# Kernel optimization log

Hardware: AMD Instinct MI355X
Metric: run time of the kernel (lower is better)

The kernel has to match this reference:

```python
import jax, jax.numpy as jnp
from jax import lax
import numpy as np
import math

B_SZ, SEQ, D_MODEL = 2, 2048, 2048
D_INNER, D_STATE, D_CONV, HEADS, P, CHUNK = 4096, 128, 4, 64, 64, 128
CONV_DIM = D_INNER + 2 * D_STATE
D_IN_PROJ = 2 * D_INNER + 2 * D_STATE + HEADS


def setup_inputs() -> dict:
    key = jax.random.key(0)
    ks = jax.random.split(key, 6)
    hidden_states = jax.random.normal(ks[0], (B_SZ, SEQ, D_MODEL), jnp.float32)
    W_in = jax.random.normal(ks[1], (D_IN_PROJ, D_MODEL), jnp.float32) * 0.02
    W_conv = jax.random.normal(ks[2], (CONV_DIM, 1, D_CONV), jnp.float32) * 0.2
    b_conv = jnp.zeros((CONV_DIM,), jnp.float32)
    A_log = jnp.log(jnp.arange(1, HEADS + 1, dtype=jnp.float32))
    D = jnp.ones((HEADS,), jnp.float32)
    # dt_bias init as in the torch module
    dt = jnp.exp(jax.random.uniform(ks[3], (HEADS,)) * (math.log(0.1) - math.log(0.001)) + math.log(0.001))
    dt = jnp.clip(dt, 1e-4, None)
    dt_bias = dt + jnp.log(-jnp.expm1(-dt))
    norm_weight = jnp.ones((D_INNER,), jnp.float32)
    W_out = jax.random.normal(ks[4], (D_MODEL, D_INNER), jnp.float32) * 0.02
    return {"hidden_states": hidden_states, "W_in": W_in, "W_conv": W_conv, "b_conv": b_conv,
            "A_log": A_log, "D": D, "dt_bias": dt_bias, "norm_weight": norm_weight, "W_out": W_out}


def _mamba2_core(hidden_states, W_in, W_conv, b_conv, A_log, D, dt_bias, norm_weight, W_out):
    Bsz, L, _ = hidden_states.shape
    NC = L // CHUNK
    zxbcdt = hidden_states @ W_in.T                         # [B,L,d_in_proj]
    z = zxbcdt[..., :D_INNER]
    xBC = zxbcdt[..., D_INNER:D_INNER + CONV_DIM]
    dt = zxbcdt[..., -HEADS:]
    # causal depthwise conv1d over sequence
    xc = jnp.swapaxes(xBC, 1, 2)                            # [B,C,L]
    xc = lax.conv_general_dilated(xc, W_conv, (1,), [(D_CONV - 1, 0)],
                                  feature_group_count=CONV_DIM,
                                  dimension_numbers=('NCH', 'OIH', 'NCH'))
    xc = xc + b_conv[None, :, None]
    xBC = jax.nn.silu(jnp.swapaxes(xc, 1, 2))               # [B,L,conv_dim]
    x = xBC[..., :D_INNER]
    Bm = xBC[..., D_INNER:D_INNER + D_STATE]                # num_groups=1
    Cm = xBC[..., -D_STATE:]
    dt = jax.nn.softplus(dt + dt_bias)                      # [B,L,H]; dt_limit (0,inf) is a no-op
    A = -jnp.exp(A_log)                                     # [H]
    # --- chunked SSD scan (chunk_size = CHUNK), same math as torch_ssm ---
    xch = x.reshape(Bsz, NC, CHUNK, HEADS, P)
    dtc = dt.reshape(Bsz, NC, CHUNK, HEADS)
    Bc = Bm.reshape(Bsz, NC, CHUNK, D_STATE)
    Cc = Cm.reshape(Bsz, NC, CHUNK, D_STATE)
    u = xch * dtc[..., None]                                # [b,c,l,h,p]
    dA = dtc * A                                            # [b,c,l,h]
    dA_cs = jnp.cumsum(dA, axis=2)                          # [b,c,l,h]
    # within-chunk causal attention-like term
    seg = dA_cs[:, :, :, None, :] - dA_cs[:, :, None, :, :] # [b,c,l,s,h]
    mask = jnp.tril(jnp.ones((CHUNK, CHUNK), bool))
    Lmat = jnp.exp(jnp.where(mask[None, None, :, :, None], seg, -jnp.inf))
    CB = jnp.einsum('bcln,bcsn->bcls', Cc, Bc)
    M = CB[..., None] * Lmat                                # [b,c,l,s,h]
    Y_diag = jnp.einsum('bclsh,bcshp->bclhp', M, u)
    # per-chunk final states
    decay_states = jnp.exp(dA_cs[:, :, -1:, :] - dA_cs)     # [b,c,l,h]
    states = jnp.einsum('bcln,bclh,bclhp->bchpn', Bc, decay_states, u)
    chunk_decay = jnp.exp(dA_cs[:, :, -1, :])               # [b,c,h]
    # inter-chunk recurrence over NC chunks
    def step(h, inp):
        st, cd = inp                                        # [b,h,p,n], [b,h]
        h_new = h * cd[:, :, None, None] + st
        return h_new, h                                     # emit state at chunk start
    sts = jnp.moveaxis(states, 1, 0)
    cds = jnp.moveaxis(chunk_decay, 1, 0)
    h0 = jnp.zeros((Bsz, HEADS, P, D_STATE), hidden_states.dtype)
    _, h_starts = lax.scan(step, h0, (sts, cds))
    h_starts = jnp.moveaxis(h_starts, 0, 1)                 # [b,c,h,p,n]
    state_decay_out = jnp.exp(dA_cs)                        # [b,c,l,h]
    Y_off = jnp.einsum('bcln,bclh,bchpn->bclhp', Cc, state_decay_out, h_starts)
    Y = Y_diag + Y_off + D[None, None, None, :, None] * xch
    y = Y.reshape(Bsz, L, D_INNER)
    # gated RMSNorm (gate first, then norm; group_size == d_inner)
    yg = y * jax.nn.silu(z)
    var = jnp.mean(yg * yg, axis=-1, keepdims=True)
    y = yg * lax.rsqrt(var + 1e-5) * norm_weight
    return y @ W_out.T


def reference(hidden_states, W_in, W_conv, b_conv, A_log, D, dt_bias, norm_weight, W_out):
    return _mamba2_core(hidden_states, W_in, W_conv, b_conv, A_log, D, dt_bias, norm_weight, W_out)
```

## Files before the change

kernel.cpp:

```cpp
#include <hip/hip_runtime.h>
#include <hip/hip_bf16.h>
#include <stdint.h>

typedef __bf16 bf16;
typedef __bf16 bf16x8 __attribute__((ext_vector_type(8)));
typedef __bf16 bf16x4 __attribute__((ext_vector_type(4)));
typedef float f32x4v __attribute__((ext_vector_type(4)));

#define SEQ    2048
#define DMODEL 2048
#define DI     4096
#define NH     64
#define PDIM   64
#define CHUNKL 128
#define NCH    16
#define CONVD  4352
#define DPROJ  8512
#define ZLD    8704
#define NTOK   4096
#define LP     136

__device__ __forceinline__ float sigmoid_f(float x){ return 1.f/(1.f+expf(-x)); }
__device__ __forceinline__ float silu_f(float x){ return x*sigmoid_f(x); }
__device__ __forceinline__ float softplus_f(float x){ return x > 20.f ? x : log1pf(expf(x)); }

__global__ __launch_bounds__(256) void cvt_all_kernel(const float* __restrict__ hs,
                                                      const float* __restrict__ W_in,
                                                      const float* __restrict__ W_out,
                                                      bf16* __restrict__ hsb,
                                                      bf16* __restrict__ winb,
                                                      bf16* __restrict__ woutb){
    int blk = blockIdx.x;
    if (blk < 8192){
        int i = (blk*256 + threadIdx.x)*4;
        float4 v = *(const float4*)&hs[i];
        bf16x4 o; o[0]=(bf16)v.x; o[1]=(bf16)v.y; o[2]=(bf16)v.z; o[3]=(bf16)v.w;
        *(bf16x4*)&hsb[i] = o;
    } else if (blk < 25600){
        int i = ((blk-8192)*256 + threadIdx.x)*4;
        int r = i >> 11;
        bf16x4 o;
        if (r < DPROJ){
            float4 v = *(const float4*)&W_in[i];
            o[0]=(bf16)v.x; o[1]=(bf16)v.y; o[2]=(bf16)v.z; o[3]=(bf16)v.w;
        } else {
            o[0]=(bf16)0.f; o[1]=(bf16)0.f; o[2]=(bf16)0.f; o[3]=(bf16)0.f;
        }
        *(bf16x4*)&winb[i] = o;
    } else {
        int i = ((blk-25600)*256 + threadIdx.x)*4;
        float4 v = *(const float4*)&W_out[i];
        bf16x4 o; o[0]=(bf16)v.x; o[1]=(bf16)v.y; o[2]=(bf16)v.z; o[3]=(bf16)v.w;
        *(bf16x4*)&woutb[i] = o;
    }
}

#define READ_A(BUFP, QM)                                                               \
    {                                                                                  \
        _Pragma("unroll")                                                              \
        for (int i=0;i<4;i++)                                                          \
            _Pragma("unroll")                                                          \
            for (int k2=0;k2<2;k2++)                                                   \
                af[i][k2] = *(const bf16x8*)&(BUFP)[aoff[i][k2] + (QM)*8192];          \
    }

#define READ_B(BUFP, QN)                                                               \
    {                                                                                  \
        _Pragma("unroll")                                                              \
        for (int nf=0;nf<2;nf++)                                                       \
            _Pragma("unroll")                                                          \
            for (int k2=0;k2<2;k2++)                                                   \
                bfr[nf][k2] = *(const bf16x8*)&(BUFP)[boff[nf][k2] + (QN)*8192];       \
    }

#define MMA_Q(QM, QN)                                                                  \
    {                                                                                  \
        __builtin_amdgcn_s_setprio(1);                                                 \
        _Pragma("unroll")                                                              \
        for (int i=0;i<4;i++)                                                          \
            _Pragma("unroll")                                                          \
            for (int nf=0;nf<2;nf++)                                                   \
                _Pragma("unroll")                                                      \
                for (int k2=0;k2<2;k2++)                                               \
                    acc[(QM)*4+i][(QN)*2+nf] = __builtin_amdgcn_mfma_f32_16x16x32_bf16( \
                        af[i][k2], bfr[nf][k2], acc[(QM)*4+i][(QN)*2+nf], 0,0,0);      \
        __builtin_amdgcn_s_setprio(0);                                                 \
    }

#define SBAR() do { __builtin_amdgcn_sched_barrier(0);                                 \
                    __builtin_amdgcn_s_barrier();                                      \
                    asm volatile("s_waitcnt lgkmcnt(0)" ::: "memory");                 \
                    __builtin_amdgcn_sched_barrier(0); } while(0)
#define EBAR() do { __builtin_amdgcn_s_barrier();                                      \
                    __builtin_amdgcn_sched_barrier(0); } while(0)

template<int MODE>
__global__ __launch_bounds__(512) void gemm256_kernel(const bf16* __restrict__ A,
                                                      const bf16* __restrict__ Bmat,
                                                      void* __restrict__ Cout,
                                                      int NXB, int NYB, int K, int ldc){
    __shared__ __align__(16) bf16 lds[2][2*16384];
    const int tid  = threadIdx.x;
    const int w    = tid >> 6;
    const int lane = tid & 63;
    const int wm   = w >> 2, wn = w & 3;

    int bid = blockIdx.x;
    int x, y, kz = 0;
    if (MODE == 3){
        kz = bid >> 5;
        int t32 = bid & 31;
        x = 32 + (t32 & 1);
        y = t32 >> 1;
    } else {
        int nb2  = (int)gridDim.x;
        int wg   = (bid & 7)*(nb2 >> 3) + (bid >> 3);
        const int SW = 8;
        int sup = wg / (SW*NYB);
        int rr  = wg % (SW*NYB);
        int x0  = sup*SW;
        int wl  = (NXB - x0 < SW) ? (NXB - x0) : SW;
        x = x0 + rr % wl;
        y = rr / wl;
    }
    const int tm = y*256, tn = x*256;

    const int KT  = (MODE==3) ? 8 : (K >> 6);
    const int kt0 = kz * KT;

    f32x4v acc[8][4];
    #pragma unroll
    for (int i=0;i<8;i++)
        #pragma unroll
        for (int j=0;j<4;j++) acc[i][j] = {0.f,0.f,0.f,0.f};
    bf16x8 af[4][2];
    bf16x8 bfr[2][2];

    const bf16* srcA[2][2];
    const bf16* srcB[2][2];
    #pragma unroll
    for (int r0h=0;r0h<2;r0h++)
        #pragma unroll
        for (int i=0;i<2;i++){
            int lr = r0h*128 + i*64 + (tid>>3);
            int growA = tm + ((lr>>6)&1)*128 + (lr>>7)*64 + (lr&63);
            int growB = tn + ((lr>>5)&3)*64 + (lr>>7)*32 + (lr&31);
            int gslot = (tid&7) ^ (lr&7);
            srcA[r0h][i] = A + (long)growA*K + gslot*8;
            srcB[r0h][i] = Bmat + (long)growB*K + gslot*8;
        }
    int aoff[4][2], boff[2][2];
    #pragma unroll
    for (int i=0;i<4;i++)
        #pragma unroll
        for (int k2=0;k2<2;k2++){
            int ra0 = wm*64 + i*16 + (lane&15);
            int slot = (k2*4 + (lane>>4)) ^ (ra0&7);
            aoff[i][k2] = ra0*64 + slot*8;
        }
    #pragma unroll
    for (int nf=0;nf<2;nf++)
        #pragma unroll
        for (int k2=0;k2<2;k2++){
            int rb0 = wn*32 + nf*16 + (lane&15);
            int slot = (k2*4 + (lane>>4)) ^ (rb0&7);
            boff[nf][k2] = 16384 + rb0*64 + slot*8;
        }

    auto stageA = [&](int buf, int t, int r0h){
        long koff = (long)(kt0 + t)*64;
        #pragma unroll
        for (int i=0;i<2;i++){
            bf16* dst = &lds[buf][0] + (size_t)(r0h*128 + i*64 + w*8)*64;
            __builtin_amdgcn_global_load_lds(
                (const __attribute__((address_space(1))) void*)(srcA[r0h][i] + koff),
                (__attribute__((address_space(3))) void*)dst, 16, 0, 0);
        }
    };
    auto stageB = [&](int buf, int t, int r0h){
        long koff = (long)(kt0 + t)*64;
        #pragma unroll
        for (int i=0;i<2;i++){
            bf16* dst = &lds[buf][16384] + (size_t)(r0h*128 + i*64 + w*8)*64;
            __builtin_amdgcn_global_load_lds(
                (const __attribute__((address_space(1))) void*)(srcB[r0h][i] + koff),
                (__attribute__((address_space(3))) void*)dst, 16, 0, 0);
        }
    };

    stageA(0, 0, 0);
    stageB(0, 0, 0);
    stageA(0, 0, 1);
    stageB(0, 0, 1);
    if (KT > 1){ stageA(1, 1, 0); stageB(1, 1, 0); }
    asm volatile("s_waitcnt vmcnt(8)" ::: "memory");
    __builtin_amdgcn_s_barrier();

    int cur = 0;
    for (int t = 0; t < KT; ++t){
        int nxt = cur ^ 1;
        const bf16* bufc = &lds[cur][0];
        READ_A(bufc, 0)
        READ_B(bufc, 0)
        if (t+1 < KT){
            stageA(nxt, t+1, 1);
            asm volatile("s_waitcnt vmcnt(6)" ::: "memory");
        } else {
            asm volatile("s_waitcnt vmcnt(0)" ::: "memory");
        }
        SBAR();
        MMA_Q(0, 0)
        READ_B(bufc, 1)
        if (t+1 < KT) stageB(nxt, t+1, 1);
        SBAR();
        MMA_Q(0, 1)
        READ_A(bufc, 1)
        READ_B(bufc, 0)
        if (t+2 < KT) stageA(cur, t+2, 0);
        SBAR();
        MMA_Q(1, 0)
        EBAR();
        READ_B(bufc, 1)
        if (t+2 < KT){
            stageB(cur, t+2, 0);
            asm volatile("s_waitcnt vmcnt(8)" ::: "memory");
        } else {
            asm volatile("s_waitcnt vmcnt(4)" ::: "memory");
        }
        SBAR();
        MMA_Q(1, 1)
        cur = nxt;
    }

    const int er = (lane>>4)*4, ec = lane&15;
    #pragma unroll
    for (int mi=0;mi<8;mi++)
        #pragma unroll
        for (int ni=0;ni<4;ni++){
            long r0 = tm + wm*128 + mi*16 + er;
            int  c0 = tn + wn*64 + ni*16 + ec;
            #pragma unroll
            for (int j=0;j<4;j++){
                float val = acc[mi][ni][j];
                if (MODE == 1){
                    ((bf16*)Cout)[(r0+j)*ldc + c0] = (bf16)val;
                } else {
                    ((float*)Cout)[((long)kz*4096 + (r0+j))*512 + (c0 - 8192)] = val;
                }
            }
        }
}

__global__ __launch_bounds__(512) void gemm256x128_kernel(const bf16* __restrict__ A,
                                                          const bf16* __restrict__ Bmat,
                                                          float* __restrict__ C,
                                                          int NXB, int NYB, int K, int ldc){
    __shared__ __align__(16) bf16 lds[3][24576];
    const int tid  = threadIdx.x;
    const int w    = tid >> 6;
    const int lane = tid & 63;
    const int wm   = w >> 2, wn = w & 3;

    int bid = blockIdx.x, nb = gridDim.x;
    int wg = (bid & 7)*(nb >> 3) + (bid >> 3);
    const int SW = 8;
    int sup = wg / (SW*NYB);
    int rr  = wg % (SW*NYB);
    int x0  = sup*SW;
    int wl  = (NXB - x0 < SW) ? (NXB - x0) : SW;
    int x   = x0 + rr % wl;
    int y   = rr / wl;
    const int tm = y*256, tn = x*128;
    const int KT = K >> 6;

    f32x4v acc[8][2];
    #pragma unroll
    for (int i=0;i<8;i++)
        #pragma unroll
        for (int j=0;j<2;j++) acc[i][j] = {0.f,0.f,0.f,0.f};
    bf16x8 af[4][2];
    bf16x8 bfr[2][2];

    const bf16* srcA[2][2];
    const bf16* srcB[2];
    #pragma unroll
    for (int r0h=0;r0h<2;r0h++)
        #pragma unroll
        for (int i=0;i<2;i++){
            int lr = r0h*128 + i*64 + (tid>>3);
            int growA = tm + ((lr>>6)&1)*128 + (lr>>7)*64 + (lr&63);
            int gslot = (tid&7) ^ (lr&7);
            srcA[r0h][i] = A + (long)growA*K + gslot*8;
        }
    #pragma unroll
    for (int i=0;i<2;i++){
        int lr = i*64 + (tid>>3);
        int growB = tn + lr;
        int gslot = (tid&7) ^ (lr&7);
        srcB[i] = Bmat + (long)growB*K + gslot*8;
    }
    int aoff[4][2], boff[2][2];
    #pragma unroll
    for (int i=0;i<4;i++)
        #pragma unroll
        for (int k2=0;k2<2;k2++){
            int ra0 = wm*64 + i*16 + (lane&15);
            int slot = (k2*4 + (lane>>4)) ^ (ra0&7);
            aoff[i][k2] = ra0*64 + slot*8;
        }
    #pragma unroll
    for (int nf=0;nf<2;nf++)
        #pragma unroll
        for (int k2=0;k2<2;k2++){
            int rb0 = wn*32 + nf*16 + (lane&15);
            int slot = (k2*4 + (lane>>4)) ^ (rb0&7);
            boff[nf][k2] = 16384 + rb0*64 + slot*8;
        }

    auto stageA = [&](int buf, int t, int r0h){
        long koff = (long)t*64;
        #pragma unroll
        for (int i=0;i<2;i++){
            bf16* dst = &lds[buf][0] + (size_t)(r0h*128 + i*64 + w*8)*64;
            __builtin_amdgcn_global_load_lds(
                (const __attribute__((address_space(1))) void*)(srcA[r0h][i] + koff),
                (__attribute__((address_space(3))) void*)dst, 16, 0, 0);
        }
    };
    auto stageB = [&](int buf, int t){
        long koff = (long)t*64;
        #pragma unroll
        for (int i=0;i<2;i++){
            bf16* dst = &lds[buf][16384] + (size_t)(i*64 + w*8)*64;
            __builtin_amdgcn_global_load_lds(
                (const __attribute__((address_space(1))) void*)(srcB[i] + koff),
                (__attribute__((address_space(3))) void*)dst, 16, 0, 0);
        }
    };

    stageA(0, 0, 0); stageA(0, 0, 1); stageB(0, 0);
    if (KT > 1){ stageA(1, 1, 0); stageA(1, 1, 1); stageB(1, 1); }
    asm volatile("s_waitcnt vmcnt(6)" ::: "memory");
    __builtin_amdgcn_s_barrier();

    int cur = 0;
    for (int t = 0; t < KT; ++t){
        int stb = cur + 2; if (stb >= 3) stb -= 3;
        const bf16* bufc = &lds[cur][0];
        READ_A(bufc, 0)
        READ_B(bufc, 0)
        if (t+2 < KT){ stageA(stb, t+2, 0); stageA(stb, t+2, 1); }
        SBAR();
        MMA_Q(0, 0)
        READ_A(bufc, 1)
        if (t+2 < KT){
            stageB(stb, t+2);
            asm volatile("s_waitcnt vmcnt(6)" ::: "memory");
        } else {
            asm volatile("s_waitcnt vmcnt(0)" ::: "memory");
        }
        SBAR();
        MMA_Q(1, 0)
        cur = (cur == 2) ? 0 : cur + 1;
    }

    const int er = (lane>>4)*4, ec = lane&15;
    #pragma unroll
    for (int mi=0;mi<8;mi++)
        #pragma unroll
        for (int ni=0;ni<2;ni++){
            long r0 = tm + wm*128 + mi*16 + er;
            int  c0 = tn + wn*32 + ni*16 + ec;
            #pragma unroll
            for (int j=0;j<4;j++)
                C[(r0+j)*ldc + c0] = acc[mi][ni][j];
        }
}

__global__ __launch_bounds__(256) void tailreduce_kernel(const float* __restrict__ p,
                                                         bf16* __restrict__ zx,
                                                         float* __restrict__ dtf){
    long i = ((long)blockIdx.x*256 + threadIdx.x)*4;
    int r = (int)(i >> 9);
    int c = (int)(i & 511);
    const long Q = (long)4096*512;
    float4 a  = *(const float4*)&p[i];
    float4 b  = *(const float4*)&p[i+Q];
    float4 cc = *(const float4*)&p[i+2*Q];
    float4 d  = *(const float4*)&p[i+3*Q];
    float s0 = a.x+b.x+cc.x+d.x, s1 = a.y+b.y+cc.y+d.y;
    float s2 = a.z+b.z+cc.z+d.z, s3 = a.w+b.w+cc.w+d.w;
    bf16x4 o; o[0]=(bf16)s0; o[1]=(bf16)s1; o[2]=(bf16)s2; o[3]=(bf16)s3;
    *(bf16x4*)&zx[(long)r*ZLD + 8192 + c] = o;
    int col = 8192 + c;
    float sv[4] = {s0,s1,s2,s3};
    #pragma unroll
    for (int j=0;j<4;j++){
        int cj = col + j;
        if (cj >= 8448 && cj < 8512) dtf[(long)r*64 + (cj-8448)] = sv[j];
    }
}

__global__ __launch_bounds__(256) void conv_silu_kernel(const bf16* __restrict__ zx,
                                                        const float* __restrict__ Wc,
                                                        const float* __restrict__ bc,
                                                        bf16* __restrict__ xc){
    int c4 = blockIdx.x*256 + threadIdx.x;
    if (c4 >= 1088) return;
    int ch = c4*4;
    int byy = blockIdx.y;
    int b = byy >> 8, t0 = (byy & 255)*8;
    float4 tap[4];
    #pragma unroll
    for (int e=0;e<4;e++) tap[e] = *(const float4*)&Wc[(ch+e)*4];
    float4 bq = *(const float4*)&bc[ch];
    float bca[4] = {bq.x, bq.y, bq.z, bq.w};
    const bf16* col = zx + (long)(b*SEQ)*ZLD + 4096 + ch;
    bf16x4 v[11];
    #pragma unroll
    for (int k=0;k<11;k++){
        int t = t0 - 3 + k;
        if (t >= 0) v[k] = *(const bf16x4*)&col[(long)t*ZLD];
        else { v[k][0]=(bf16)0.f; v[k][1]=(bf16)0.f; v[k][2]=(bf16)0.f; v[k][3]=(bf16)0.f; }
    }
    #pragma unroll
    for (int j=0;j<8;j++){
        bf16x4 o;
        #pragma unroll
        for (int e=0;e<4;e++){
            float acc = bca[e] + (float)v[j][e]*tap[e].x + (float)v[j+1][e]*tap[e].y
                               + (float)v[j+2][e]*tap[e].z + (float)v[j+3][e]*tap[e].w;
            o[e] = (bf16)silu_f(acc);
        }
        *(bf16x4*)&xc[(long)(b*SEQ + t0 + j)*CONVD + ch] = o;
    }
}

__global__ __launch_bounds__(256) void dtcum_kernel(const float* __restrict__ dtf,
                                                    const float* __restrict__ A_log,
                                                    const float* __restrict__ dt_bias,
                                                    float* __restrict__ dtv,
                                                    float* __restrict__ dacs,
                                                    float* __restrict__ cdec){
    int wid  = (blockIdx.x*256 + threadIdx.x) >> 6;
    int lane = threadIdx.x & 63;
    int h  = wid & 63, bc = wid >> 6;
    int b  = bc >> 4,  c  = bc & 15;
    float Ah   = -expf(A_log[h]);
    float bias = dt_bias[h];
    long tok0 = (long)(b*SEQ + c*CHUNKL);
    int l0 = lane*2;
    float d0 = softplus_f(dtf[(tok0+l0)*64 + h] + bias);
    float d1 = softplus_f(dtf[(tok0+l0+1)*64 + h] + bias);
    float s = (d0 + d1)*Ah;
    #pragma unroll
    for (int off=1; off<64; off<<=1){
        float t = __shfl_up(s, off, 64);
        if (lane >= off) s += t;
    }
    long base_h = (long)wid*128;
    float cs1 = s;
    float cs0 = s - d1*Ah;
    dtv[base_h+l0]   = d0;  dtv[base_h+l0+1]  = d1;
    dacs[base_h+l0]  = cs0; dacs[base_h+l0+1] = cs1;
    if (lane == 63) cdec[wid] = expf(cs1);
}

__global__ __launch_bounds__(256) void cb_mfma_kernel(const bf16* __restrict__ xc,
                                                      float* __restrict__ cb){
    __shared__ __align__(16) bf16 A1[128*LP];
    __shared__ __align__(16) bf16 B1[128*LP];
    int blk = blockIdx.x;  int b = blk>>4, c = blk&15;
    int tid = threadIdx.x;
    const int w = tid >> 6, lane = tid & 63;
    long tok0 = (long)(b*SEQ + c*CHUNKL);
    int l = tid>>1, n0 = (tid&1)*64;
    const bf16* crow = xc + tok0*CONVD + (long)l*CONVD;
    #pragma unroll
    for (int v=0;v<8;v++){
        *(bf16x8*)&A1[l*LP + n0 + v*8] = *(const bf16x8*)&crow[4224 + n0 + v*8];
        *(bf16x8*)&B1[l*LP + n0 + v*8] = *(const bf16x8*)&crow[4096 + n0 + v*8];
    }
    __syncthreads();
    f32x4v acc[2][8];
    #pragma unroll
    for (int mi=0;mi<2;mi++)
        #pragma unroll
        for (int ni=0;ni<8;ni++) acc[mi][ni] = {0.f,0.f,0.f,0.f};
    #pragma unroll
    for (int kk=0; kk<128; kk+=32){
        bf16x8 afr[2], bfr2[8];
        #pragma unroll
        for (int mi=0;mi<2;mi++)
            afr[mi] = *(const bf16x8*)&A1[(w*32 + mi*16 + (lane&15))*LP + kk + (lane>>4)*8];
        #pragma unroll
        for (int ni=0;ni<8;ni++)
            bfr2[ni] = *(const bf16x8*)&B1[(ni*16 + (lane&15))*LP + kk + (lane>>4)*8];
        #pragma unroll
        for (int mi=0;mi<2;mi++)
            #pragma unroll
            for (int ni=0;ni<8;ni++)
                acc[mi][ni] = __builtin_amdgcn_mfma_f32_16x16x32_bf16(afr[mi], bfr2[ni], acc[mi][ni], 0,0,0);
    }
    float* out = cb + (long)blk*16384;
    #pragma unroll
    for (int mi=0;mi<2;mi++)
        #pragma unroll
        for (int ni=0;ni<8;ni++){
            int r0 = w*32 + mi*16 + (lane>>4)*4;
            int c0 = ni*16 + (lane&15);
            #pragma unroll
            for (int j=0;j<4;j++) out[(long)(r0+j)*128 + c0] = acc[mi][ni][j];
        }
}

__global__ __launch_bounds__(256) void states_mfma_kernel(const bf16* __restrict__ xc,
                                                          const float* __restrict__ dtv,
                                                          const float* __restrict__ dacs,
                                                          bf16* __restrict__ states){
    __shared__ __align__(16) bf16 A1[64*LP];
    __shared__ __align__(16) bf16 B1[128*LP];
    __shared__ float wgtl[128];
    int blk = blockIdx.x;
    int h = blk & 63, bc = blk >> 6;
    int b = bc >> 4, c = bc & 15;
    int tid = threadIdx.x;
    const int w = tid >> 6, lane = tid & 63;
    long tok0 = (long)(b*SEQ + c*CHUNKL);
    long base_h = (long)blk*128;
    float cs_last = dacs[base_h + 127];
    if (tid < 128) wgtl[tid] = dtv[base_h+tid] * expf(cs_last - dacs[base_h+tid]);
    __syncthreads();
    #pragma unroll
    for (int t=0;t<4;t++){
        int l = (tid>>3) + t*32;
        int p0 = (tid&7)*8;
        bf16x8 xv = *(const bf16x8*)&xc[(tok0+l)*CONVD + h*64 + p0];
        float wv = wgtl[l];
        #pragma unroll
        for (int e=0;e<8;e++) A1[(p0+e)*LP + l] = (bf16)((float)xv[e]*wv);
    }
    {
        int l = tid>>1, n0 = (tid&1)*64;
        const bf16* brow = xc + (tok0+l)*CONVD + 4096;
        #pragma unroll
        for (int v=0;v<8;v++){
            bf16x8 bv = *(const bf16x8*)&brow[n0 + v*8];
            #pragma unroll
            for (int e=0;e<8;e++) B1[(n0+v*8+e)*LP + l] = bv[e];
        }
    }
    __syncthreads();
    f32x4v acc[8];
    #pragma unroll
    for (int ni=0;ni<8;ni++) acc[ni] = {0.f,0.f,0.f,0.f};
    #pragma unroll
    for (int kk=0; kk<128; kk+=32){
        bf16x8 afr = *(const bf16x8*)&A1[(w*16 + (lane&15))*LP + kk + (lane>>4)*8];
        #pragma unroll
        for (int ni=0;ni<8;ni++){
            bf16x8 bfr2 = *(const bf16x8*)&B1[(ni*16 + (lane&15))*LP + kk + (lane>>4)*8];
            acc[ni] = __builtin_amdgcn_mfma_f32_16x16x32_bf16(afr, bfr2, acc[ni], 0,0,0);
        }
    }
    bf16* out = states + (long)blk*8192;
    #pragma unroll
    for (int ni=0;ni<8;ni++){
        int p0 = w*16 + (lane>>4)*4;
        int n  = ni*16 + (lane&15);
        #pragma unroll
        for (int j=0;j<4;j++) out[(long)(p0+j)*128 + n] = (bf16)acc[ni][j];
    }
}

__global__ __launch_bounds__(256) void scan_kernel(const bf16* __restrict__ states,
                                                   const float* __restrict__ cdec,
                                                   bf16* __restrict__ hst){
    long gid = (long)blockIdx.x*256 + threadIdx.x;
    int n = gid & 127;
    int p = (gid >> 7) & 63;
    int h = (gid >> 13) & 63;
    int b = (int)(gid >> 19);
    float hrun = 0.f;
    for (int c=0;c<16;c++){
        long idx = ((((long)(b*16 + c)*64 + h)*64 + p)*128) + n;
        hst[idx] = (bf16)hrun;
        hrun = hrun * cdec[(b*16+c)*64 + h] + (float)states[idx];
    }
}

__global__ __launch_bounds__(256) void yfused_kernel(const bf16* __restrict__ xc,
                                                     const float* __restrict__ cb,
                                                     const bf16* __restrict__ hst,
                                                     const float* __restrict__ dtv,
                                                     const float* __restrict__ dacs,
                                                     bf16* __restrict__ Ybf){
    __shared__ __align__(16) bf16 A1[128*LP];
    __shared__ __align__(16) bf16 B1[64*LP];
    __shared__ float csl[128];
    int blk = blockIdx.x;
    int h = blk & 63, bc = blk >> 6;
    int b = bc >> 4, c = bc & 15;
    int tid = threadIdx.x;
    const int w = tid >> 6, lane = tid & 63;
    long tok0 = (long)(b*SEQ + c*CHUNKL);
    long base_h = (long)blk*128;
    if (tid < 128) csl[tid] = dacs[base_h + tid];
    __syncthreads();
    {
        int l = tid>>1, s0 = (tid&1)*64;
        float el = csl[l];
        const float* cbrow = cb + (long)bc*16384 + (long)l*128 + s0;
        #pragma unroll 8
        for (int j=0;j<64;j++){
            int s = s0 + j;
            float v = (s <= l) ? cbrow[j]*expf(el - csl[s]) : 0.f;
            A1[l*LP + s] = (bf16)v;
        }
    }
    #pragma unroll
    for (int t=0;t<4;t++){
        int s = (tid>>3) + t*32;
        int p0 = (tid&7)*8;
        bf16x8 xv = *(const bf16x8*)&xc[(tok0+s)*CONVD + h*64 + p0];
        float wv = dtv[base_h + s];
        #pragma unroll
        for (int e=0;e<8;e++) B1[(p0+e)*LP + s] = (bf16)((float)xv[e]*wv);
    }
    __syncthreads();
    f32x4v acc[2][4];
    #pragma unroll
    for (int mi=0;mi<2;mi++)
        #pragma unroll
        for (int ni=0;ni<4;ni++) acc[mi][ni] = {0.f,0.f,0.f,0.f};
    #pragma unroll
    for (int kk=0; kk<128; kk+=32){
        bf16x8 afr[2], bfr2[4];
        #pragma unroll
        for (int mi=0;mi<2;mi++)
            afr[mi] = *(const bf16x8*)&A1[(w*32 + mi*16 + (lane&15))*LP + kk + (lane>>4)*8];
        #pragma unroll
        for (int ni=0;ni<4;ni++)
            bfr2[ni] = *(const bf16x8*)&B1[(ni*16 + (lane&15))*LP + kk + (lane>>4)*8];
        #pragma unroll
        for (int mi=0;mi<2;mi++)
            #pragma unroll
            for (int ni=0;ni<4;ni++)
                acc[mi][ni] = __builtin_amdgcn_mfma_f32_16x16x32_bf16(afr[mi], bfr2[ni], acc[mi][ni], 0,0,0);
    }
    __syncthreads();
    {
        int l = tid>>1, n0 = (tid&1)*64;
        float e1 = expf(csl[l]);
        const bf16* crow = xc + (tok0+l)*CONVD + 4224;
        #pragma unroll
        for (int v=0;v<8;v++){
            bf16x8 cv = *(const bf16x8*)&crow[n0 + v*8];
            bf16x8 o;
            #pragma unroll
            for (int e=0;e<8;e++) o[e] = (bf16)((float)cv[e]*e1);
            *(bf16x8*)&A1[l*LP + n0 + v*8] = o;
        }
    }
    {
        int p = tid>>2, n0 = (tid&3)*32;
        const bf16* hrow = hst + (long)blk*8192 + (long)p*128 + n0;
        #pragma unroll
        for (int v=0;v<4;v++)
            *(bf16x8*)&B1[p*LP + n0 + v*8] = *(const bf16x8*)&hrow[v*8];
    }
    __syncthreads();
    #pragma unroll
    for (int kk=0; kk<128; kk+=32){
        bf16x8 afr[2], bfr2[4];
        #pragma unroll
        for (int mi=0;mi<2;mi++)
            afr[mi] = *(const bf16x8*)&A1[(w*32 + mi*16 + (lane&15))*LP + kk + (lane>>4)*8];
        #pragma unroll
        for (int ni=0;ni<4;ni++)
            bfr2[ni] = *(const bf16x8*)&B1[(ni*16 + (lane&15))*LP + kk + (lane>>4)*8];
        #pragma unroll
        for (int mi=0;mi<2;mi++)
            #pragma unroll
            for (int ni=0;ni<4;ni++)
                acc[mi][ni] = __builtin_amdgcn_mfma_f32_16x16x32_bf16(afr[mi], bfr2[ni], acc[mi][ni], 0,0,0);
    }
    #pragma unroll
    for (int mi=0;mi<2;mi++)
        #pragma unroll
        for (int ni=0;ni<4;ni++){
            int l0 = w*32 + mi*16 + (lane>>4)*4;
            int p  = ni*16 + (lane&15);
            #pragma unroll
            for (int j=0;j<4;j++)
                Ybf[(tok0 + l0 + j)*DI + h*64 + p] = (bf16)acc[mi][ni][j];
        }
}

__global__ __launch_bounds__(256) void gatenorm_kernel(const bf16* __restrict__ Ybf,
                                                       const bf16* __restrict__ zx,
                                                       const bf16* __restrict__ xc,
                                                       const float* __restrict__ Dp,
                                                       const float* __restrict__ nw,
                                                       bf16* __restrict__ ybn){
    __shared__ float red[4];
    int tok = blockIdx.x, tid = threadIdx.x;
    const bf16* yrow = Ybf + (long)tok*DI;
    const bf16* zrow = zx  + (long)tok*ZLD;
    const bf16* xrow = xc  + (long)tok*CONVD;
    float yg[16];
    float ss = 0.f;
    #pragma unroll
    for (int k=0;k<2;k++){
        int d = (tid + k*256)*8;
        bf16x8 yv = *(const bf16x8*)&yrow[d];
        bf16x8 zv = *(const bf16x8*)&zrow[d];
        bf16x8 xv = *(const bf16x8*)&xrow[d];
        float dh = Dp[d>>6];
        #pragma unroll
        for (int e=0;e<8;e++){
            float yy = (float)yv[e] + dh*(float)xv[e];
            float g = yy*silu_f((float)zv[e]);
            yg[k*8+e] = g;
            ss += g*g;
        }
    }
    #pragma unroll
    for (int off=32; off>0; off>>=1) ss += __shfl_down(ss, off, 64);
    if ((tid & 63) == 0) red[tid>>6] = ss;
    __syncthreads();
    float tot = red[0]+red[1]+red[2]+red[3];
    float scale = rsqrtf(tot/(float)DI + 1e-5f);
    #pragma unroll
    for (int k=0;k<2;k++){
        int d = (tid + k*256)*8;
        float4 w0 = *(const float4*)&nw[d];
        float4 w1 = *(const float4*)&nw[d+4];
        float wv[8] = {w0.x,w0.y,w0.z,w0.w,w1.x,w1.y,w1.z,w1.w};
        bf16x8 o;
        #pragma unroll
        for (int e=0;e<8;e++) o[e] = (bf16)(yg[k*8+e]*scale*wv[e]);
        *(bf16x8*)&ybn[(long)tok*DI + d] = o;
    }
}

extern "C" void kernel_launch(void* const* d_in, const int* in_sizes, int n_in,
                              void* d_out, int out_size, void* d_ws, size_t ws_size,
                              hipStream_t stream){
    const float* hs      = (const float*)d_in[0];
    const float* W_in    = (const float*)d_in[1];
    const float* W_conv  = (const float*)d_in[2];
    const float* b_conv  = (const float*)d_in[3];
    const float* A_log   = (const float*)d_in[4];
    const float* Dp      = (const float*)d_in[5];
    const float* dt_bias = (const float*)d_in[6];
    const float* nw      = (const float*)d_in[7];
    const float* W_out   = (const float*)d_in[8];
    float* out = (float*)d_out;

    char* ws = (char*)d_ws;
    const size_t OFF_ZX    = 0;
    const size_t OFF_DTF   = 71303168;
    const size_t OFF_XC    = 72351744;
    const size_t OFF_DTV   = 108003328;
    const size_t OFF_DACS  = 109051904;
    const size_t OFF_CDEC  = 110100480;
    const size_t OFF_CB    = 110108672;
    const size_t OFF_SLOTA = 112205824;
    const size_t OFF_SLOTB = 179314688;
    const size_t OFF_WOUTB = 212869120;

    bf16*  zx    = (bf16*)(ws + OFF_ZX);
    float* dtf   = (float*)(ws + OFF_DTF);
    bf16*  xc    = (bf16*)(ws + OFF_XC);
    float* dtv   = (float*)(ws + OFF_DTV);
    float* dacs  = (float*)(ws + OFF_DACS);
    float* cdec  = (float*)(ws + OFF_CDEC);
    float* cbuf  = (float*)(ws + OFF_CB);
    bf16*  hsb   = (bf16*)(ws + OFF_SLOTA);
    bf16*  winb  = (bf16*)(ws + OFF_SLOTA + 16777216);
    bf16*  states= (bf16*)(ws + OFF_SLOTA);
    bf16*  Ybf   = (bf16*)(ws + OFF_SLOTA);
    float* tpart = (float*)(ws + OFF_SLOTB);
    bf16*  hst   = (bf16*)(ws + OFF_SLOTB);
    bf16*  ybn   = (bf16*)(ws + OFF_SLOTB);
    bf16*  woutb = (bf16*)(ws + OFF_WOUTB);

    cvt_all_kernel<<<33792, 256, 0, stream>>>(hs, W_in, W_out, hsb, winb, woutb);

    gemm256_kernel<1><<<512, 512, 0, stream>>>(hsb, winb, (void*)zx,
                                               32, 16, DMODEL, ZLD);
    gemm256_kernel<3><<<128, 512, 0, stream>>>(hsb, winb, (void*)tpart,
                                               34, 16, DMODEL, ZLD);
    tailreduce_kernel<<<2048, 256, 0, stream>>>(tpart, zx, dtf);

    conv_silu_kernel<<<dim3(5, 512), 256, 0, stream>>>(zx, W_conv, b_conv, xc);
    dtcum_kernel<<<512, 256, 0, stream>>>(dtf, A_log, dt_bias, dtv, dacs, cdec);
    cb_mfma_kernel<<<32, 256, 0, stream>>>(xc, cbuf);
    states_mfma_kernel<<<2048, 256, 0, stream>>>(xc, dtv, dacs, states);
    scan_kernel<<<4096, 256, 0, stream>>>(states, cdec, hst);
    yfused_kernel<<<2048, 256, 0, stream>>>(xc, cbuf, hst, dtv, dacs, Ybf);
    gatenorm_kernel<<<4096, 256, 0, stream>>>(Ybf, zx, xc, Dp, nw, ybn);

    gemm256x128_kernel<<<256, 512, 0, stream>>>(ybn, woutb, out, 16, 16, DI, DMODEL);
}
```

Before: 438.1 us.

## Merge in-proj GEMM launches and restructure K-loop into two-phase pipeline

Combines the main in-projection GEMM and the split-K tail GEMM into one 640-block launch, using the block index to pick the role. This removes one launch and lets the tail blocks run alongside the main tiles. The K-loop is also reworked: both B fragments are read up front into separate registers, and each iteration has two barrier phases instead of four, with the next-next stage's loads issued after the MMAs. This cuts barrier count but raises register pressure and changes how load waits overlap with compute.

```diff
diff --git a/kernel.cpp b/kernel.cpp
--- a/kernel.cpp
+++ b/kernel.cpp
@@ -64,16 +64,16 @@
                 af[i][k2] = *(const bf16x8*)&(BUFP)[aoff[i][k2] + (QM)*8192];          \
     }
 
-#define READ_B(BUFP, QN)                                                               \
+#define READ_B(BUFP, QN, BFR)                                                          \
     {                                                                                  \
         _Pragma("unroll")                                                              \
         for (int nf=0;nf<2;nf++)                                                       \
             _Pragma("unroll")                                                          \
             for (int k2=0;k2<2;k2++)                                                   \
-                bfr[nf][k2] = *(const bf16x8*)&(BUFP)[boff[nf][k2] + (QN)*8192];       \
-    }
-
-#define MMA_Q(QM, QN)                                                                  \
+                BFR[nf][k2] = *(const bf16x8*)&(BUFP)[boff[nf][k2] + (QN)*8192];       \
+    }
+
+#define MMA_Q(QM, QN, BFR)                                                             \
     {                                                                                  \
         __builtin_amdgcn_s_setprio(1);                                                 \
         _Pragma("unroll")                                                              \
@@ -83,7 +83,7 @@
                 _Pragma("unroll")                                                      \
                 for (int k2=0;k2<2;k2++)                                               \
                     acc[(QM)*4+i][(QN)*2+nf] = __builtin_amdgcn_mfma_f32_16x16x32_bf16( \
-                        af[i][k2], bfr[nf][k2], acc[(QM)*4+i][(QN)*2+nf], 0,0,0);      \
+                        af[i][k2], BFR[nf][k2], acc[(QM)*4+i][(QN)*2+nf], 0,0,0);      \
         __builtin_amdgcn_s_setprio(0);                                                 \
     }
 
@@ -91,14 +91,12 @@
                     __builtin_amdgcn_s_barrier();                                      \
                     asm volatile("s_waitcnt lgkmcnt(0)" ::: "memory");                 \
                     __builtin_amdgcn_sched_barrier(0); } while(0)
-#define EBAR() do { __builtin_amdgcn_s_barrier();                                      \
-                    __builtin_amdgcn_sched_barrier(0); } while(0)
-
-template<int MODE>
-__global__ __launch_bounds__(512) void gemm256_kernel(const bf16* __restrict__ A,
-                                                      const bf16* __restrict__ Bmat,
-                                                      void* __restrict__ Cout,
-                                                      int NXB, int NYB, int K, int ldc){
+
+__global__ __launch_bounds__(512) void gemm1_kernel(const bf16* __restrict__ A,
+                                                    const bf16* __restrict__ Bmat,
+                                                    bf16* __restrict__ Cz,
+                                                    float* __restrict__ tpart,
+                                                    int NXB, int NYB, int K){
     __shared__ __align__(16) bf16 lds[2][2*16384];
     const int tid  = threadIdx.x;
     const int w    = tid >> 6;
@@ -106,15 +104,16 @@
     const int wm   = w >> 2, wn = w & 3;
 
     int bid = blockIdx.x;
-    int x, y, kz = 0;
-    if (MODE == 3){
+    int x, y, kz = 0, KT, kt0;
+    if (bid < 128){
         kz = bid >> 5;
         int t32 = bid & 31;
         x = 32 + (t32 & 1);
         y = t32 >> 1;
+        KT = 8; kt0 = kz*8;
     } else {
-        int nb2  = (int)gridDim.x;
-        int wg   = (bid & 7)*(nb2 >> 3) + (bid >> 3);
+        int bid2 = bid - 128;
+        int wg   = (bid2 & 7)*64 + (bid2 >> 3);
         const int SW = 8;
         int sup = wg / (SW*NYB);
         int rr  = wg % (SW*NYB);
@@ -122,11 +121,9 @@
         int wl  = (NXB - x0 < SW) ? (NXB - x0) : SW;
         x = x0 + rr % wl;
         y = rr / wl;
+        KT = K >> 6; kt0 = 0;
     }
     const int tm = y*256, tn = x*256;
-
-    const int KT  = (MODE==3) ? 8 : (K >> 6);
-    const int kt0 = kz * KT;
 
     f32x4v acc[8][4];
     #pragma unroll
@@ -134,7 +131,7 @@
         #pragma unroll
         for (int j=0;j<4;j++) acc[i][j] = {0.f,0.f,0.f,0.f};
     bf16x8 af[4][2];
-    bf16x8 bfr[2][2];
+    bf16x8 bfr0[2][2], bfr1[2][2];
 
     const bf16* srcA[2][2];
     const bf16* srcB[2][2];
@@ -188,11 +185,8 @@
         }
     };
 
-    stageA(0, 0, 0);
-    stageB(0, 0, 0);
-    stageA(0, 0, 1);
-    stageB(0, 0, 1);
-    if (KT > 1){ stageA(1, 1, 0); stageB(1, 1, 0); }
+    stageA(0, 0, 0); stageB(0, 0, 0); stageA(0, 0, 1); stageB(0, 0, 1);
+    if (KT > 1){ stageA(1, 1, 0); stageB(1, 1, 0); stageA(1, 1, 1); stageB(1, 1, 1); }
     asm volatile("s_waitcnt vmcnt(8)" ::: "memory");
     __builtin_amdgcn_s_barrier();
 
@@ -201,34 +195,21 @@
         int nxt = cur ^ 1;
         const bf16* bufc = &lds[cur][0];
         READ_A(bufc, 0)
-        READ_B(bufc, 0)
-        if (t+1 < KT){
-            stageA(nxt, t+1, 1);
-            asm volatile("s_waitcnt vmcnt(6)" ::: "memory");
-        } else {
-            asm volatile("s_waitcnt vmcnt(0)" ::: "memory");
-        }
+        READ_B(bufc, 0, bfr0)
+        READ_B(bufc, 1, bfr1)
+        if (t+1 < KT){ asm volatile("s_waitcnt vmcnt(8)" ::: "memory"); }
+        else         { asm volatile("s_waitcnt vmcnt(0)" ::: "memory"); }
         SBAR();
-        MMA_Q(0, 0)
-        READ_B(bufc, 1)
-        if (t+1 < KT) stageB(nxt, t+1, 1);
+        MMA_Q(0, 0, bfr0)
+        MMA_Q(0, 1, bfr1)
+        __builtin_amdgcn_sched_barrier(0);
+        if (t+2 < KT){ stageA(cur, t+2, 0); stageB(cur, t+2, 0); }
+        READ_A(bufc, 1)
         SBAR();
-        MMA_Q(0, 1)
-        READ_A(bufc, 1)
-        READ_B(bufc, 0)
-        if (t+2 < KT) stageA(cur, t+2, 0);
-        SBAR();
-        MMA_Q(1, 0)
-        EBAR();
-        READ_B(bufc, 1)
-        if (t+2 < KT){
-            stageB(cur, t+2, 0);
-            asm volatile("s_waitcnt vmcnt(8)" ::: "memory");
-        } else {
-            asm volatile("s_waitcnt vmcnt(4)" ::: "memory");
-        }
-        SBAR();
-        MMA_Q(1, 1)
+        MMA_Q(1, 0, bfr0)
+        MMA_Q(1, 1, bfr1)
+        __builtin_amdgcn_sched_barrier(0);
+        if (t+2 < KT){ stageA(cur, t+2, 1); stageB(cur, t+2, 1); }
         cur = nxt;
     }
 
@@ -242,10 +223,10 @@
             #pragma unroll
             for (int j=0;j<4;j++){
                 float val = acc[mi][ni][j];
-                if (MODE == 1){
-                    ((bf16*)Cout)[(r0+j)*ldc + c0] = (bf16)val;
+                if (x < 32){
+                    Cz[(r0+j)*ZLD + c0] = (bf16)val;
                 } else {
-                    ((float*)Cout)[((long)kz*4096 + (r0+j))*512 + (c0 - 8192)] = val;
+                    tpart[((long)kz*4096 + (r0+j))*512 + (c0 - 8192)] = val;
                 }
             }
         }
@@ -348,10 +329,10 @@
         int stb = cur + 2; if (stb >= 3) stb -= 3;
         const bf16* bufc = &lds[cur][0];
         READ_A(bufc, 0)
-        READ_B(bufc, 0)
+        READ_B(bufc, 0, bfr)
         if (t+2 < KT){ stageA(stb, t+2, 0); stageA(stb, t+2, 1); }
         SBAR();
-        MMA_Q(0, 0)
+        MMA_Q(0, 0, bfr)
         READ_A(bufc, 1)
         if (t+2 < KT){
             stageB(stb, t+2);
@@ -360,7 +341,7 @@
             asm volatile("s_waitcnt vmcnt(0)" ::: "memory");
         }
         SBAR();
-        MMA_Q(1, 0)
+        MMA_Q(1, 0, bfr)
         cur = (cur == 2) ? 0 : cur + 1;
     }
 
@@ -788,10 +769,7 @@
 
     cvt_all_kernel<<<33792, 256, 0, stream>>>(hs, W_in, W_out, hsb, winb, woutb);
 
-    gemm256_kernel<1><<<512, 512, 0, stream>>>(hsb, winb, (void*)zx,
-                                               32, 16, DMODEL, ZLD);
-    gemm256_kernel<3><<<128, 512, 0, stream>>>(hsb, winb, (void*)tpart,
-                                               34, 16, DMODEL, ZLD);
+    gemm1_kernel<<<640, 512, 0, stream>>>(hsb, winb, zx, tpart, 32, 16, DMODEL);
     tailreduce_kernel<<<2048, 256, 0, stream>>>(tpart, zx, dtf);
 
     conv_silu_kernel<<<dim3(5, 512), 256, 0, stream>>>(zx, W_conv, b_conv, xc);
```

Result: no change. 431.3 us (-1.6%).
